# Kernel optimization log

Measured on AMD Instinct MI355X. Metric: run time of the kernel, lower is better.

## Reference

```python
import jax, jax.numpy as jnp
import numpy as np

S = 768           # sentence length
V_WORD = 30000    # len(words_dict) + len(SPECIAL_TOKENS)
V_POS = 64        # len(poses_dict) + len(SPECIAL_TOKENS)
WORD_EMB = 100
POS_EMB = 28
EMB = WORD_EMB + POS_EMB   # 128, LSTM input size
H = 256                    # lstm_h_dim
MLP = 128                  # mlp_h_dim


def setup_inputs() -> dict:
    key = jax.random.key(0)
    ks = iter(jax.random.split(key, 48))

    def n(shape, scale=0.05):
        return jax.random.normal(next(ks), shape, dtype=jnp.float32) * scale

    inp = {
        "word_idx_tensor": jax.random.randint(next(ks), (S,), 0, V_WORD),
        "pos_idx_tensor": jax.random.randint(next(ks), (S,), 0, V_POS),
        "sentence_len": S,
        "W_word": n((V_WORD, WORD_EMB), 0.1),
        "W_pos": n((V_POS, POS_EMB), 0.1),
    }
    # 2-layer bidirectional LSTM, PyTorch weight layout (gates i,f,g,o stacked)
    for l, in_dim in ((0, EMB), (1, 2 * H)):
        for d in ("f", "b"):
            inp[f"Wih_l{l}{d}"] = n((4 * H, in_dim))
            inp[f"Whh_l{l}{d}"] = n((4 * H, H))
            inp[f"bih_l{l}{d}"] = n((4 * H,))
            inp[f"bhh_l{l}{d}"] = n((4 * H,))
    # edge scorer: Linear(1024 -> 128), Tanh, Linear(128 -> 1)
    inp["W1"] = n((MLP, 4 * H))   # 2*lstm_layers*lstm_h_dim = 1024
    inp["b1"] = n((MLP,))
    inp["W2"] = n((1, MLP))
    inp["b2"] = n((1,))
    return inp


def _lstm_dir(x, Wih, Whh, bih, bhh, reverse):
    # x: [S, in_dim] -> hidden sequence [S, H] for one direction
    Hn = Whh.shape[1]
    gx = x @ Wih.T + bih + bhh  # precompute input contribution [S, 4H]

    def step(carry, g0):
        h, c = carry
        g = g0 + h @ Whh.T
        i, f, gc, o = jnp.split(g, 4)
        c = jax.nn.sigmoid(f) * c + jax.nn.sigmoid(i) * jnp.tanh(gc)
        h = jax.nn.sigmoid(o) * jnp.tanh(c)
        return (h, c), h

    init = (jnp.zeros((Hn,), x.dtype), jnp.zeros((Hn,), x.dtype))
    _, hs = jax.lax.scan(step, init, gx, reverse=reverse)
    return hs  # ys are in original time order for reverse=True as well


def _bilstm(x, Wf, Uf, bf, cf, Wb, Ub, bb, cb):
    return jnp.concatenate(
        [_lstm_dir(x, Wf, Uf, bf, cf, False), _lstm_dir(x, Wb, Ub, bb, cb, True)],
        axis=1,
    )


def reference(word_idx_tensor, pos_idx_tensor, sentence_len, W_word, W_pos,
              Wih_l0f, Whh_l0f, bih_l0f, bhh_l0f, Wih_l0b, Whh_l0b, bih_l0b, bhh_l0b,
              Wih_l1f, Whh_l1f, bih_l1f, bhh_l1f, Wih_l1b, Whh_l1b, bih_l1b, bhh_l1b,
              W1, b1, W2, b2):
    # embeddings, concat along feature dim -> [S, EMB]
    x = jnp.concatenate([W_word[word_idx_tensor], W_pos[pos_idx_tensor]], axis=1)
    # 2-layer BiLSTM (eval mode: inter-layer dropout inactive) -> [S, 2H]
    h = _bilstm(x, Wih_l0f, Whh_l0f, bih_l0f, bhh_l0f, Wih_l0b, Whh_l0b, bih_l0b, bhh_l0b)
    h = _bilstm(h, Wih_l1f, Whh_l1f, bih_l1f, bhh_l1f, Wih_l1b, Whh_l1b, bih_l1b, bhh_l1b)
    # pairwise scorer: Linear(cat(h_i, h_j)) == A h_i + B h_j, batched over all pairs
    half = W1.shape[1] // 2
    hA = h @ W1[:, :half].T   # [S, MLP] head part
    hB = h @ W1[:, half:].T   # [S, MLP] modifier part
    t = jnp.tanh(hA[:, None, :] + hB[None, :, :] + b1)  # [S, S, MLP]
    scores = t @ W2[0] + b2[0]                          # [S, S]
    eye = jnp.eye(scores.shape[0], dtype=bool)
    return jnp.where(eye, jnp.float32(0.0), scores)     # diagonal forced to 0
```

## Files before the change

### kernel.cpp

```cpp
#include <hip/hip_runtime.h>

#define S_LEN 768
#define EMB   128
#define HDIM  256
#define GATES 1024
#define MLP   128
#define SENT  0xAAAAAAAAu

__global__ void embed_kernel(const int* __restrict__ widx, const int* __restrict__ pidx,
                             const float* __restrict__ Ww, const float* __restrict__ Wp,
                             float* __restrict__ x0) {
    int t = blockIdx.x, k = threadIdx.x;
    float v;
    if (k < 100) v = Ww[widx[t] * 100 + k];
    else         v = Wp[pidx[t] * 28 + (k - 100)];
    x0[t * EMB + k] = v;
}

__global__ __launch_bounds__(256) void gemm_bias(
    const float* __restrict__ A, int lda,
    const float* __restrict__ B, int ldb,
    const float* __restrict__ bias1, const float* __restrict__ bias2,
    float* __restrict__ C, int ldc, int K) {
    __shared__ float As[32][65];
    __shared__ float Bs[32][65];
    const int t  = threadIdx.x;
    const int m0 = blockIdx.x * 64, n0 = blockIdx.y * 64;
    const int tm = t >> 4, tn = t & 15;
    float acc[4][4];
#pragma unroll
    for (int i = 0; i < 4; ++i)
#pragma unroll
        for (int j = 0; j < 4; ++j) acc[i][j] = 0.f;

    for (int k0 = 0; k0 < K; k0 += 32) {
#pragma unroll
        for (int l = 0; l < 8; ++l) {
            int idx = t + l * 256;
            int m = idx >> 5, kk = idx & 31;
            As[kk][m] = A[(m0 + m) * lda + k0 + kk];
            Bs[kk][m] = B[(n0 + m) * ldb + k0 + kk];
        }
        __syncthreads();
#pragma unroll
        for (int kk = 0; kk < 32; ++kk) {
            float a4[4], b4[4];
#pragma unroll
            for (int i = 0; i < 4; ++i) a4[i] = As[kk][tm * 4 + i];
#pragma unroll
            for (int j = 0; j < 4; ++j) b4[j] = Bs[kk][tn * 4 + j];
#pragma unroll
            for (int i = 0; i < 4; ++i)
#pragma unroll
                for (int j = 0; j < 4; ++j)
                    acc[i][j] = fmaf(a4[i], b4[j], acc[i][j]);
        }
        __syncthreads();
    }
    float bb[4];
#pragma unroll
    for (int j = 0; j < 4; ++j) {
        int n = n0 + tn * 4 + j;
        bb[j] = (bias1 ? bias1[n] : 0.f) + (bias2 ? bias2[n] : 0.f);
    }
#pragma unroll
    for (int i = 0; i < 4; ++i) {
        int m = m0 + tm * 4 + i;
        float4 o;
        o.x = acc[i][0] + bb[0];
        o.y = acc[i][1] + bb[1];
        o.z = acc[i][2] + bb[2];
        o.w = acc[i][3] + bb[3];
        *(float4*)(&C[m * ldc + n0 + tn * 4]) = o;
    }
}

__global__ __launch_bounds__(256, 1) void lstm_rec(
    const float* __restrict__ WhhF, const float* __restrict__ WhhB,
    const float* __restrict__ gxF, const float* __restrict__ gxB,
    float* __restrict__ hOut)
{
    __shared__ float4 wlds[8 * 256];
    __shared__ float  hps[256];
    __shared__ float  gl[32];
    const int tid = threadIdx.x;
    const int dir = blockIdx.x & 1;
    const int sl  = blockIdx.x >> 1;
    const float* __restrict__ Whh = dir ? WhhB : WhhF;
    const float* __restrict__ gx  = dir ? gxB  : gxF;
    unsigned int* hbits = (unsigned int*)hOut;

    const int lr = tid >> 3, q = tid & 7;
    const int grow = (lr >> 3) * 256 + sl * 8 + (lr & 7);

    {
        const float4* Wg = (const float4*)(Whh + grow * HDIM + q * 32);
#pragma unroll
        for (int i = 0; i < 8; ++i) wlds[i * 256 + tid] = Wg[i];
    }

    float creg = 0.f;
    float gval = (q == 0) ? gx[(dir ? (S_LEN - 1) : 0) * GATES + grow] : 0.f;

    for (int t = 0; t < S_LEN; ++t) {
        const int tp = dir ? (S_LEN - 1 - t) : t;
        {
            float hv;
            if (t > 0) {
                const int tpp = dir ? (tp + 1) : (tp - 1);
                unsigned int b;
                do {
                    b = __hip_atomic_load(&hbits[tpp * 512 + dir * HDIM + tid],
                                          __ATOMIC_RELAXED, __HIP_MEMORY_SCOPE_AGENT);
                } while (b == SENT);
                hv = __uint_as_float(b);
            } else {
                hv = 0.f;
            }
            const int qq = tid >> 5, ii = (tid >> 2) & 7;
            hps[(qq * 8 + (ii ^ qq)) * 4 + (tid & 3)] = hv;
        }
        __syncthreads();

        float gnext = 0.f;
        if (q == 0 && t + 1 < S_LEN) {
            const int tpn = dir ? (tp - 1) : (tp + 1);
            gnext = gx[tpn * GATES + grow];
        }

        const float4* hp4 = (const float4*)hps;
        float4 a = {0.f, 0.f, 0.f, 0.f};
#pragma unroll
        for (int i = 0; i < 8; ++i) {
            float4 wv = wlds[i * 256 + tid];
            float4 hv = hp4[q * 8 + (i ^ q)];
            a.x = fmaf(wv.x, hv.x, a.x);
            a.y = fmaf(wv.y, hv.y, a.y);
            a.z = fmaf(wv.z, hv.z, a.z);
            a.w = fmaf(wv.w, hv.w, a.w);
        }
        float acc = (a.x + a.y) + (a.z + a.w);
        acc += __shfl_xor(acc, 1);
        acc += __shfl_xor(acc, 2);
        acc += __shfl_xor(acc, 4);
        if (q == 0) gl[lr] = acc + gval;
        __syncthreads();

        if (tid < 8) {
            float gi = gl[tid], gf = gl[8 + tid], gg = gl[16 + tid], go = gl[24 + tid];
            float si = __fdividef(1.f, 1.f + __expf(-gi));
            float sf = __fdividef(1.f, 1.f + __expf(-gf));
            float so = __fdividef(1.f, 1.f + __expf(-go));
            float eg = __expf(2.f * gg);
            float tg = 1.f - __fdividef(2.f, eg + 1.f);
            creg = fmaf(sf, creg, si * tg);
            float ec = __expf(2.f * creg);
            float tc = 1.f - __fdividef(2.f, ec + 1.f);
            float hv = so * tc;
            unsigned int ob = __float_as_uint(hv);
            if (ob == SENT) ob ^= 1u;
            __hip_atomic_store(&hbits[tp * 512 + dir * HDIM + sl * 8 + tid], ob,
                               __ATOMIC_RELAXED, __HIP_MEMORY_SCOPE_AGENT);
        }
        gval = gnext;
    }
}

__device__ __forceinline__ float tanh_fast(float x) {
    float e = __expf(2.f * x);
    return 1.f - __fdividef(2.f, e + 1.f);
}

__global__ __launch_bounds__(256) void scorer(
    const float* __restrict__ hA, const float* __restrict__ hB,
    const float* __restrict__ w2, const float* __restrict__ b2,
    float* __restrict__ out) {
    __shared__ float Al[32][129];
    __shared__ float Bl[32][129];
    __shared__ float w2s[128];
    const int t  = threadIdx.x;
    const int i0 = blockIdx.x * 32, j0 = blockIdx.y * 32;
    for (int idx = t; idx < 32 * 128; idx += 256) {
        int r = idx >> 7, k = idx & 127;
        Al[r][k] = hA[(i0 + r) * MLP + k];
        Bl[r][k] = hB[(j0 + r) * MLP + k];
    }
    if (t < 128) w2s[t] = w2[t];
    __syncthreads();

    const int j = t & 31, i2 = t >> 5;
    const float base = b2[0];
    float acc0 = base, acc1 = base, acc2 = base, acc3 = base;
#pragma unroll 4
    for (int k = 0; k < 128; ++k) {
        float bv = Bl[j][k];
        float wv = w2s[k];
        float y0 = Al[i2 * 4 + 0][k] + bv;
        float y1 = Al[i2 * 4 + 1][k] + bv;
        float y2 = Al[i2 * 4 + 2][k] + bv;
        float y3 = Al[i2 * 4 + 3][k] + bv;
        acc0 = fmaf(wv, tanh_fast(y0), acc0);
        acc1 = fmaf(wv, tanh_fast(y1), acc1);
        acc2 = fmaf(wv, tanh_fast(y2), acc2);
        acc3 = fmaf(wv, tanh_fast(y3), acc3);
    }
    const int jj = j0 + j;
    float accs[4] = {acc0, acc1, acc2, acc3};
#pragma unroll
    for (int ii = 0; ii < 4; ++ii) {
        int i = i0 + i2 * 4 + ii;
        out[i * S_LEN + jj] = (i == jj) ? 0.f : accs[ii];
    }
}

extern "C" void kernel_launch(void* const* d_in, const int* in_sizes, int n_in,
                              void* d_out, int out_size, void* d_ws, size_t ws_size,
                              hipStream_t stream) {
    (void)in_sizes; (void)n_in; (void)out_size; (void)ws_size;
    const int*   widx  = (const int*)d_in[0];
    const int*   pidx  = (const int*)d_in[1];
    const float* Ww    = (const float*)d_in[3];
    const float* Wp    = (const float*)d_in[4];
    const float* Wih0f = (const float*)d_in[5];
    const float* Whh0f = (const float*)d_in[6];
    const float* bih0f = (const float*)d_in[7];
    const float* bhh0f = (const float*)d_in[8];
    const float* Wih0b = (const float*)d_in[9];
    const float* Whh0b = (const float*)d_in[10];
    const float* bih0b = (const float*)d_in[11];
    const float* bhh0b = (const float*)d_in[12];
    const float* Wih1f = (const float*)d_in[13];
    const float* Whh1f = (const float*)d_in[14];
    const float* bih1f = (const float*)d_in[15];
    const float* bhh1f = (const float*)d_in[16];
    const float* Wih1b = (const float*)d_in[17];
    const float* Whh1b = (const float*)d_in[18];
    const float* bih1b = (const float*)d_in[19];
    const float* bhh1b = (const float*)d_in[20];
    const float* W1    = (const float*)d_in[21];
    const float* b1    = (const float*)d_in[22];
    const float* W2    = (const float*)d_in[23];
    const float* b2    = (const float*)d_in[24];

    float* ws  = (float*)d_ws;
    float* x0  = ws;
    float* h0  = x0 + S_LEN * EMB;
    float* h1  = h0 + S_LEN * 512;
    float* gxf = h1 + S_LEN * 512;
    float* gxb = gxf + S_LEN * GATES;
    float* hA  = gxb + S_LEN * GATES;
    float* hB  = hA + S_LEN * MLP;

    hipMemsetAsync(h0, 0xAA, 2 * S_LEN * 512 * sizeof(float), stream);

    embed_kernel<<<S_LEN, EMB, 0, stream>>>(widx, pidx, Ww, Wp, x0);

    dim3 gg(12, 16);
    gemm_bias<<<gg, 256, 0, stream>>>(x0, EMB, Wih0f, EMB, bih0f, bhh0f, gxf, GATES, EMB);
    gemm_bias<<<gg, 256, 0, stream>>>(x0, EMB, Wih0b, EMB, bih0b, bhh0b, gxb, GATES, EMB);
    lstm_rec<<<64, 256, 0, stream>>>(Whh0f, Whh0b, gxf, gxb, h0);

    gemm_bias<<<gg, 256, 0, stream>>>(h0, 512, Wih1f, 512, bih1f, bhh1f, gxf, GATES, 512);
    gemm_bias<<<gg, 256, 0, stream>>>(h0, 512, Wih1b, 512, bih1b, bhh1b, gxb, GATES, 512);
    lstm_rec<<<64, 256, 0, stream>>>(Whh1f, Whh1b, gxf, gxb, h1);

    dim3 ga(12, 2);
    gemm_bias<<<ga, 256, 0, stream>>>(h1, 512, W1,       1024, b1,      nullptr, hA, MLP, 512);
    gemm_bias<<<ga, 256, 0, stream>>>(h1, 512, W1 + 512, 1024, nullptr, nullptr, hB, MLP, 512);

    dim3 gs(24, 24);
    scorer<<<gs, 256, 0, stream>>>(hA, hB, W2, b2, (float*)d_out);
}
```

Baseline: 2.854 ms.

## Vectorize h polling, double-buffer LDS h, and replace gate sync with shuffles

Each recurrent step now has 64 threads poll the previous hidden state with 16-byte cache-bypassing loads instead of 256 scalar atomic loads. A spin limit falls back to per-element atomic loads. The h buffer in LDS is double-buffered, and the gate rows are remapped so all four gates of one hidden unit sit in the same 32-lane half, which lets cross-lane shuffles replace the second __syncthreads and the gl LDS staging. The aim is to cut per-step synchronisation latency on the serial LSTM critical path. The risks are inline-asm cache-coherence subtleties and an unconventional shuffle pattern, given the 64-wide wavefront.

```diff
diff --git a/kernel.cpp b/kernel.cpp
--- a/kernel.cpp
+++ b/kernel.cpp
@@ -6,6 +6,13 @@
 #define GATES 1024
 #define MLP   128
 #define SENT  0xAAAAAAAAu
+
+__device__ __forceinline__ float4 ld16_sc01(const void* p) {
+    float4 v;
+    asm volatile("global_load_dwordx4 %0, %1, off sc0 sc1\n\ts_waitcnt vmcnt(0)"
+                 : "=v"(v) : "v"(p) : "memory");
+    return v;
+}
 
 __global__ void embed_kernel(const int* __restrict__ widx, const int* __restrict__ pidx,
                              const float* __restrict__ Ww, const float* __restrict__ Wp,
@@ -81,8 +88,7 @@
     float* __restrict__ hOut)
 {
     __shared__ float4 wlds[8 * 256];
-    __shared__ float  hps[256];
-    __shared__ float  gl[32];
+    __shared__ float4 hps[2][64];
     const int tid = threadIdx.x;
     const int dir = blockIdx.x & 1;
     const int sl  = blockIdx.x >> 1;
@@ -91,7 +97,7 @@
     unsigned int* hbits = (unsigned int*)hOut;
 
     const int lr = tid >> 3, q = tid & 7;
-    const int grow = (lr >> 3) * 256 + sl * 8 + (lr & 7);
+    const int grow = (lr & 3) * 256 + sl * 8 + (lr >> 2);
 
     {
         const float4* Wg = (const float4*)(Whh + grow * HDIM + q * 32);
@@ -104,21 +110,33 @@
 
     for (int t = 0; t < S_LEN; ++t) {
         const int tp = dir ? (S_LEN - 1 - t) : t;
-        {
-            float hv;
+        const int buf = t & 1;
+        if (tid < 64) {
+            float4 b = {0.f, 0.f, 0.f, 0.f};
             if (t > 0) {
                 const int tpp = dir ? (tp + 1) : (tp - 1);
-                unsigned int b;
-                do {
-                    b = __hip_atomic_load(&hbits[tpp * 512 + dir * HDIM + tid],
-                                          __ATOMIC_RELAXED, __HIP_MEMORY_SCOPE_AGENT);
-                } while (b == SENT);
-                hv = __uint_as_float(b);
-            } else {
-                hv = 0.f;
+                const unsigned int* pw = hbits + tpp * 512 + dir * HDIM + tid * 4;
+                int spin = 0;
+                for (;;) {
+                    b = ld16_sc01(pw);
+                    if (__float_as_uint(b.x) != SENT && __float_as_uint(b.y) != SENT &&
+                        __float_as_uint(b.z) != SENT && __float_as_uint(b.w) != SENT)
+                        break;
+                    if (++spin >= 1024) {
+                        float* bb = &b.x;
+#pragma unroll
+                        for (int k = 0; k < 4; ++k) {
+                            unsigned int v = __float_as_uint(bb[k]);
+                            while (v == SENT)
+                                v = __hip_atomic_load(pw + k, __ATOMIC_RELAXED,
+                                                      __HIP_MEMORY_SCOPE_AGENT);
+                            bb[k] = __uint_as_float(v);
+                        }
+                        break;
+                    }
+                }
             }
-            const int qq = tid >> 5, ii = (tid >> 2) & 7;
-            hps[(qq * 8 + (ii ^ qq)) * 4 + (tid & 3)] = hv;
+            hps[buf][8 * (tid >> 3) + ((tid & 7) ^ (tid >> 3))] = b;
         }
         __syncthreads();
 
@@ -128,12 +146,12 @@
             gnext = gx[tpn * GATES + grow];
         }
 
-        const float4* hp4 = (const float4*)hps;
+        const float4* hb = hps[buf];
         float4 a = {0.f, 0.f, 0.f, 0.f};
 #pragma unroll
         for (int i = 0; i < 8; ++i) {
             float4 wv = wlds[i * 256 + tid];
-            float4 hv = hp4[q * 8 + (i ^ q)];
+            float4 hv = hb[8 * q + (i ^ q)];
             a.x = fmaf(wv.x, hv.x, a.x);
             a.y = fmaf(wv.y, hv.y, a.y);
             a.z = fmaf(wv.z, hv.z, a.z);
@@ -143,11 +161,15 @@
         acc += __shfl_xor(acc, 1);
         acc += __shfl_xor(acc, 2);
         acc += __shfl_xor(acc, 4);
-        if (q == 0) gl[lr] = acc + gval;
-        __syncthreads();
-
-        if (tid < 8) {
-            float gi = gl[tid], gf = gl[8 + tid], gg = gl[16 + tid], go = gl[24 + tid];
+        if (q == 0) acc += gval;
+
+        const int base = tid & 32;
+        float gi = __shfl(acc, base + 0);
+        float gf = __shfl(acc, base + 8);
+        float gg = __shfl(acc, base + 16);
+        float go = __shfl(acc, base + 24);
+
+        if ((tid & 31) == 0) {
             float si = __fdividef(1.f, 1.f + __expf(-gi));
             float sf = __fdividef(1.f, 1.f + __expf(-gf));
             float so = __fdividef(1.f, 1.f + __expf(-go));
@@ -159,7 +181,8 @@
             float hv = so * tc;
             unsigned int ob = __float_as_uint(hv);
             if (ob == SENT) ob ^= 1u;
-            __hip_atomic_store(&hbits[tp * 512 + dir * HDIM + sl * 8 + tid], ob,
+            const int e = tid >> 5;
+            __hip_atomic_store(&hbits[tp * 512 + dir * HDIM + sl * 8 + e], ob,
                                __ATOMIC_RELAXED, __HIP_MEMORY_SCOPE_AGENT);
         }
         gval = gnext;
```

Measured after the change: 4.023 ms. 1.41x slower.

## Halve LSTM recurrence blocks, double rows per block, wave-local gate reduction

Applied to the files above, without the earlier changes.

The recurrent LSTM kernel now runs 16 hidden units per block instead of 8, so each direction uses 16 blocks rather than 32 and the cross-block spin-wait has fewer participants. The gate values for a unit now sit in a single wavefront and are gathered with shuffles, which removes the second __syncthreads and the shared gate buffer. The h vector is double-buffered in LDS, and polling adds s_sleep. In exchange each thread does 16 float4 FMAs per step instead of 8 and needs 64KB of dynamic LDS for the weights, so per-step compute grows.

```diff
diff --git a/kernel.cpp b/kernel.cpp
--- a/kernel.cpp
+++ b/kernel.cpp
@@ -80,9 +80,9 @@
     const float* __restrict__ gxF, const float* __restrict__ gxB,
     float* __restrict__ hOut)
 {
-    __shared__ float4 wlds[8 * 256];
-    __shared__ float  hps[256];
-    __shared__ float  gl[32];
+    extern __shared__ float4 dyn[];
+    float4* wlds = dyn;
+    float4* hps  = dyn + 16 * 256;
     const int tid = threadIdx.x;
     const int dir = blockIdx.x & 1;
     const int sl  = blockIdx.x >> 1;
@@ -90,13 +90,13 @@
     const float* __restrict__ gx  = dir ? gxB  : gxF;
     unsigned int* hbits = (unsigned int*)hOut;
 
-    const int lr = tid >> 3, q = tid & 7;
-    const int grow = (lr >> 3) * 256 + sl * 8 + (lr & 7);
+    const int e = tid >> 4, g = (tid >> 2) & 3, q = tid & 3;
+    const int grow = g * 256 + sl * 16 + e;
 
     {
-        const float4* Wg = (const float4*)(Whh + grow * HDIM + q * 32);
-#pragma unroll
-        for (int i = 0; i < 8; ++i) wlds[i * 256 + tid] = Wg[i];
+        const float4* Wg = (const float4*)(Whh + grow * HDIM + q * 64);
+#pragma unroll
+        for (int i = 0; i < 16; ++i) wlds[i * 256 + tid] = Wg[i];
     }
 
     float creg = 0.f;
@@ -104,21 +104,24 @@
 
     for (int t = 0; t < S_LEN; ++t) {
         const int tp = dir ? (S_LEN - 1 - t) : t;
+        const int buf = t & 1;
         {
-            float hv;
+            float hv = 0.f;
             if (t > 0) {
                 const int tpp = dir ? (tp + 1) : (tp - 1);
-                unsigned int b;
-                do {
-                    b = __hip_atomic_load(&hbits[tpp * 512 + dir * HDIM + tid],
-                                          __ATOMIC_RELAXED, __HIP_MEMORY_SCOPE_AGENT);
-                } while (b == SENT);
-                hv = __uint_as_float(b);
-            } else {
-                hv = 0.f;
+                const unsigned int* pw = hbits + tpp * 512 + dir * HDIM + tid;
+                unsigned int v = __hip_atomic_load(pw, __ATOMIC_RELAXED,
+                                                   __HIP_MEMORY_SCOPE_AGENT);
+                while (v == SENT) {
+                    __builtin_amdgcn_s_sleep(1);
+                    v = __hip_atomic_load(pw, __ATOMIC_RELAXED,
+                                          __HIP_MEMORY_SCOPE_AGENT);
+                }
+                hv = __uint_as_float(v);
             }
-            const int qq = tid >> 5, ii = (tid >> 2) & 7;
-            hps[(qq * 8 + (ii ^ qq)) * 4 + (tid & 3)] = hv;
+            const int j = tid >> 2;
+            const int jp = (j & 48) | ((j + (j >> 4)) & 15);
+            ((float*)&hps[buf * 64 + jp])[tid & 3] = hv;
         }
         __syncthreads();
 
@@ -128,12 +131,12 @@
             gnext = gx[tpn * GATES + grow];
         }
 
-        const float4* hp4 = (const float4*)hps;
+        const float4* hb = hps + buf * 64;
         float4 a = {0.f, 0.f, 0.f, 0.f};
 #pragma unroll
-        for (int i = 0; i < 8; ++i) {
+        for (int i = 0; i < 16; ++i) {
             float4 wv = wlds[i * 256 + tid];
-            float4 hv = hp4[q * 8 + (i ^ q)];
+            float4 hv = hb[(q << 4) | ((i + q) & 15)];
             a.x = fmaf(wv.x, hv.x, a.x);
             a.y = fmaf(wv.y, hv.y, a.y);
             a.z = fmaf(wv.z, hv.z, a.z);
@@ -142,12 +145,15 @@
         float acc = (a.x + a.y) + (a.z + a.w);
         acc += __shfl_xor(acc, 1);
         acc += __shfl_xor(acc, 2);
-        acc += __shfl_xor(acc, 4);
-        if (q == 0) gl[lr] = acc + gval;
-        __syncthreads();
-
-        if (tid < 8) {
-            float gi = gl[tid], gf = gl[8 + tid], gg = gl[16 + tid], go = gl[24 + tid];
+        if (q == 0) acc += gval;
+
+        const int base = (tid & 63) & 48;
+        float gi = __shfl(acc, base + 0);
+        float gf = __shfl(acc, base + 4);
+        float gg = __shfl(acc, base + 8);
+        float go = __shfl(acc, base + 12);
+
+        if ((tid & 15) == 0) {
             float si = __fdividef(1.f, 1.f + __expf(-gi));
             float sf = __fdividef(1.f, 1.f + __expf(-gf));
             float so = __fdividef(1.f, 1.f + __expf(-go));
@@ -159,7 +165,7 @@
             float hv = so * tc;
             unsigned int ob = __float_as_uint(hv);
             if (ob == SENT) ob ^= 1u;
-            __hip_atomic_store(&hbits[tp * 512 + dir * HDIM + sl * 8 + tid], ob,
+            __hip_atomic_store(&hbits[tp * 512 + dir * HDIM + sl * 16 + e], ob,
                                __ATOMIC_RELAXED, __HIP_MEMORY_SCOPE_AGENT);
         }
         gval = gnext;
@@ -251,6 +257,10 @@
     float* hA  = gxb + S_LEN * GATES;
     float* hB  = hA + S_LEN * MLP;
 
+    const int lstm_lds = (16 * 256 + 128) * sizeof(float4);
+    hipFuncSetAttribute((const void*)lstm_rec,
+                        hipFuncAttributeMaxDynamicSharedMemorySize, lstm_lds);
+
     hipMemsetAsync(h0, 0xAA, 2 * S_LEN * 512 * sizeof(float), stream);
 
     embed_kernel<<<S_LEN, EMB, 0, stream>>>(widx, pidx, Ww, Wp, x0);
@@ -258,11 +268,11 @@
     dim3 gg(12, 16);
     gemm_bias<<<gg, 256, 0, stream>>>(x0, EMB, Wih0f, EMB, bih0f, bhh0f, gxf, GATES, EMB);
     gemm_bias<<<gg, 256, 0, stream>>>(x0, EMB, Wih0b, EMB, bih0b, bhh0b, gxb, GATES, EMB);
-    lstm_rec<<<64, 256, 0, stream>>>(Whh0f, Whh0b, gxf, gxb, h0);
+    lstm_rec<<<32, 256, lstm_lds, stream>>>(Whh0f, Whh0b, gxf, gxb, h0);
 
     gemm_bias<<<gg, 256, 0, stream>>>(h0, 512, Wih1f, 512, bih1f, bhh1f, gxf, GATES, 512);
     gemm_bias<<<gg, 256, 0, stream>>>(h0, 512, Wih1b, 512, bih1b, bhh1b, gxb, GATES, 512);
-    lstm_rec<<<64, 256, 0, stream>>>(Whh1f, Whh1b, gxf, gxb, h1);
+    lstm_rec<<<32, 256, lstm_lds, stream>>>(Whh1f, Whh1b, gxf, gxb, h1);
 
     dim3 ga(12, 2);
     gemm_bias<<<ga, 256, 0, stream>>>(h1, 512, W1,       1024, b1,      nullptr, hA, MLP, 512);
```

New measurement: 3.654 ms. 1.28x slower.
